# Optimization experiments

Hardware: AMD Instinct MI355X
Metric: run time of the kernel (lower is better)

## Reference

```python
import jax, jax.numpy as jnp
import numpy as np

H, KVH, HD, DM = 32, 8, 128, 4096  # attention heads, kv heads, head_dim, hidden


def _rope_tables(batch, seq, head_dim):
    # standard RoPE tables, flattened per token to match varlen layout
    inv_freq = 1.0 / (10000.0 ** (np.arange(0, head_dim, 2, dtype=np.float32) / head_dim))
    pos = np.arange(seq, dtype=np.float32)
    freqs = np.outer(pos, inv_freq)                      # [S, HD/2]
    emb = np.concatenate([freqs, freqs], axis=-1)        # [S, HD]
    cos = np.tile(np.cos(emb), (batch, 1))               # [B*S, HD]
    sin = np.tile(np.sin(emb), (batch, 1))
    return jnp.asarray(cos), jnp.asarray(sin)


def setup_inputs() -> dict:
    key = jax.random.key(0)
    k1, k2 = jax.random.split(key)
    B, S = 2, 1024
    hidden_states = jax.random.normal(k1, (B * S, DM), dtype=jnp.float32) * 0.02
    w_qkv = jax.random.normal(k2, (DM, (H + 2 * KVH) * HD), dtype=jnp.float32) * 0.02
    cos, sin = _rope_tables(B, S, HD)
    return {"hidden_states": hidden_states, "w_qkv": w_qkv, "cos": cos,
            "sin": sin, "batch_size": B, "seq_len": S}


def _rotate_half(x):
    half = x.shape[-1] // 2
    return jnp.concatenate([-x[..., half:], x[..., :half]], axis=-1)


def reference(hidden_states, w_qkv, cos, sin, batch_size, seq_len):
    B, S = batch_size, seq_len
    T = B * S
    n_rep = H // KVH
    scale = 1.0 / jnp.sqrt(jnp.asarray(HD, hidden_states.dtype))

    qkv = hidden_states @ w_qkv                           # [T, (H+2*KVH)*HD]
    q = qkv[:, : H * HD].reshape(T, H, HD)
    k = qkv[:, H * HD : (H + KVH) * HD].reshape(T, KVH, HD)
    v = qkv[:, (H + KVH) * HD :].reshape(T, KVH, HD)

    # RoPE (rotary half) on q and k
    c, s = cos[:, None, :], sin[:, None, :]
    q = q * c + _rotate_half(q) * s
    k = k * c + _rotate_half(k) * s

    # prefill SDPA branch: reshape to [B, heads, S, HD], GQA repeat on kv heads
    q = q.reshape(B, S, H, HD).transpose(0, 2, 1, 3)      # [B,H,S,HD]
    k = k.reshape(B, S, KVH, HD).transpose(0, 2, 1, 3)
    v = v.reshape(B, S, KVH, HD).transpose(0, 2, 1, 3)
    k = jnp.repeat(k, n_rep, axis=1)                      # [B,H,S,HD]
    v = jnp.repeat(v, n_rep, axis=1)

    scores = jnp.einsum("bhqd,bhkd->bhqk", q, k) * scale  # [B,H,S,S]
    causal = jnp.tril(jnp.ones((S, S), dtype=bool))
    scores = jnp.where(causal, scores, jnp.asarray(-jnp.inf, scores.dtype))
    probs = jax.nn.softmax(scores, axis=-1)
    attn = jnp.einsum("bhqk,bhkd->bhqd", probs, v)        # [B,H,S,HD]

    # postprocess_attention_output: transpose back and flatten tokens
    attn = attn.transpose(0, 2, 1, 3).reshape(T, H * HD)  # [T, H*HD]
    return attn
```

## Files before the change

### kernel.cpp

```cpp
#include <hip/hip_runtime.h>
#include <hip/hip_bf16.h>
#include <stdint.h>

constexpr int NH   = 32;
constexpr int NKVH = 8;
constexpr int HD   = 128;
constexpr int DM   = 4096;
constexpr int B    = 2;
constexpr int S    = 1024;
constexpr int T    = B * S;
constexpr int QKVN = (NH + 2 * NKVH) * HD;
constexpr int KOFF = NH * HD;
constexpr int VOFF = (NH + NKVH) * HD;

typedef float floatx4 __attribute__((ext_vector_type(4)));
typedef floatx4 floatx4_a __attribute__((may_alias));
typedef __bf16 bf16x8 __attribute__((ext_vector_type(8)));
typedef bf16x8 bf16x8_a __attribute__((may_alias));
typedef __bf16 bf16_a __attribute__((may_alias));

__device__ __forceinline__ void gload_lds16(const void* g, void* l) {
  __builtin_amdgcn_global_load_lds(
      (const __attribute__((address_space(1))) void*)g,
      (__attribute__((address_space(3))) void*)l, 16, 0, 0);
}

__global__ __launch_bounds__(256) void convert_a(const float* __restrict__ A,
                                                 __bf16* __restrict__ A16) {
  const size_t i = (size_t)(blockIdx.x * 256 + threadIdx.x) * 8;
  floatx4 v0 = *(const floatx4_a*)(A + i);
  floatx4 v1 = *(const floatx4_a*)(A + i + 4);
  bf16x8 o;
#pragma unroll
  for (int e = 0; e < 4; ++e) {
    o[e] = (__bf16)v0[e];
    o[e + 4] = (__bf16)v1[e];
  }
  *(bf16x8_a*)(A16 + i) = o;
}

__global__ __launch_bounds__(256) void transpose_w(
    const float* __restrict__ W, __bf16* __restrict__ WT) {
  __shared__ __align__(16) __bf16 ls[64][72];
  const int k0 = blockIdx.x * 64;
  const int n0 = blockIdx.y * 64;
  const int tx = threadIdx.x & 15, ty = threadIdx.x >> 4;
#pragma unroll
  for (int rr = 0; rr < 4; ++rr) {
    const int k = ty + rr * 16;
    floatx4 v = *(const floatx4_a*)(W + (size_t)(k0 + k) * QKVN + n0 + tx * 4);
#pragma unroll
    for (int e = 0; e < 4; ++e) ls[tx * 4 + e][k] = (__bf16)v[e];
  }
  __syncthreads();
#pragma unroll
  for (int it = 0; it < 2; ++it) {
    const int n = (threadIdx.x >> 3) + it * 32;
    const int c = threadIdx.x & 7;
    bf16x8 o = *(const bf16x8_a*)(&ls[n][c * 8]);
    *(bf16x8_a*)(WT + (size_t)(n0 + n) * DM + k0 + c * 8) = o;
  }
}

__global__ __launch_bounds__(256) void gemm_mfma(
    const __bf16* __restrict__ A16, const __bf16* __restrict__ W16T,
    float* __restrict__ C) {
  __shared__ __align__(16) __bf16 Asig[128 * 64];
  __shared__ __align__(16) __bf16 Bsig[128 * 64];

  const int tid = threadIdx.x;
  const int lane = tid & 63, w = tid >> 6;
  const int l15 = lane & 15, g = lane >> 4;
  const int r7 = l15 & 7;
  const int m0 = blockIdx.x * 128;
  const int n0 = blockIdx.y * 128;
  const int wrbase = (w >> 1) * 64, wcbase = (w & 1) * 64;

  const int srow = tid >> 3;
  const int sce = ((tid & 7) ^ (srow & 7)) << 3;
  const __bf16* agp = A16 + (size_t)(m0 + srow) * DM + sce;
  const __bf16* bgp = W16T + (size_t)(n0 + srow) * DM + sce;
  char* al = (char*)Asig + w * 1024;
  char* bl = (char*)Bsig + w * 1024;

  const char* Abase = (const char*)Asig + (wrbase + l15) * 128;
  const char* Bbase = (const char*)Bsig + (wcbase + l15) * 128;

  floatx4 acc[4][4];
#pragma unroll
  for (int i = 0; i < 4; ++i)
#pragma unroll
    for (int j = 0; j < 4; ++j) acc[i][j] = (floatx4){0.f, 0.f, 0.f, 0.f};

  for (int kk = 0; kk < DM; kk += 64) {
    __syncthreads();
#pragma unroll
    for (int j = 0; j < 4; ++j) {
      gload_lds16(agp + kk + (size_t)(32 * j) * DM, al + j * 4096);
      gload_lds16(bgp + kk + (size_t)(32 * j) * DM, bl + j * 4096);
    }
    __syncthreads();

#pragma unroll
    for (int kh = 0; kh < 2; ++kh) {
      const int sw = (((kh << 2) | g) ^ r7) << 4;
      bf16x8 af[4], bf[4];
#pragma unroll
      for (int i = 0; i < 4; ++i) {
        af[i] = *(const bf16x8_a*)(Abase + i * 2048 + sw);
        bf[i] = *(const bf16x8_a*)(Bbase + i * 2048 + sw);
      }
#pragma unroll
      for (int i = 0; i < 4; ++i)
#pragma unroll
        for (int j = 0; j < 4; ++j)
          acc[i][j] = __builtin_amdgcn_mfma_f32_16x16x32_bf16(af[i], bf[j],
                                                              acc[i][j], 0, 0, 0);
    }
  }

#pragma unroll
  for (int i = 0; i < 4; ++i)
#pragma unroll
    for (int j = 0; j < 4; ++j)
#pragma unroll
      for (int ri = 0; ri < 4; ++ri)
        C[(size_t)(m0 + wrbase + i * 16 + g * 4 + ri) * QKVN + n0 + wcbase +
          j * 16 + l15] = acc[i][j][ri];
}

__global__ __launch_bounds__(256) void gemm_naive(
    const float* __restrict__ A, const float* __restrict__ W,
    float* __restrict__ C) {
  __shared__ float As[16][65];
  __shared__ float Bs[16][64];
  const int tid = threadIdx.x;
  const int tx = tid & 15, ty = tid >> 4;
  const int m0 = blockIdx.y * 64, n0 = blockIdx.x * 64;
  const int sm = tid >> 2, sk4 = (tid & 3) * 4;
  const int bk = tid >> 4, bn4 = (tid & 15) * 4;
  float acc[4][4];
#pragma unroll
  for (int i = 0; i < 4; ++i)
#pragma unroll
    for (int j = 0; j < 4; ++j) acc[i][j] = 0.f;
  for (int kk = 0; kk < DM; kk += 16) {
    __syncthreads();
    floatx4 va = *(const floatx4_a*)(A + (size_t)(m0 + sm) * DM + kk + sk4);
#pragma unroll
    for (int e = 0; e < 4; ++e) As[sk4 + e][sm] = va[e];
    floatx4 vb = *(const floatx4_a*)(W + (size_t)(kk + bk) * QKVN + n0 + bn4);
    *(floatx4*)&Bs[bk][bn4] = vb;
    __syncthreads();
#pragma unroll
    for (int k = 0; k < 16; ++k) {
      float a[4], b[4];
#pragma unroll
      for (int e = 0; e < 4; ++e) a[e] = As[k][ty * 4 + e];
#pragma unroll
      for (int e = 0; e < 4; ++e) b[e] = Bs[k][tx * 4 + e];
#pragma unroll
      for (int i = 0; i < 4; ++i)
#pragma unroll
        for (int j = 0; j < 4; ++j) acc[i][j] += a[i] * b[j];
    }
  }
#pragma unroll
  for (int i = 0; i < 4; ++i)
#pragma unroll
    for (int j = 0; j < 4; ++j)
      C[(size_t)(m0 + ty * 4 + i) * QKVN + n0 + tx * 4 + j] = acc[i][j];
}

__global__ __launch_bounds__(256) void attn_mfma(
    const float* __restrict__ qkv, const float* __restrict__ cosp,
    const float* __restrict__ sinp, float* __restrict__ out) {
  __shared__ __align__(16) char Ksh[32 * 128 * 2];
  __shared__ __align__(16) char Vsh[128 * 32 * 2];
  __shared__ __align__(16) char Psh[4][16 * 32 * 2];

  const int tid = threadIdx.x;
  const int lane = tid & 63, wave = tid >> 6;
  const int raw = (int)blockIdx.x;
  const int qb_raw = raw & 63;
  const int qb = ((raw >> 8) & 1) ? (63 - qb_raw) : qb_raw;
  const int kvh = (raw >> 6) & 7;
  const int b = raw >> 9;
  const int q0 = qb * 16;
  const int h = kvh * 4 + wave;
  const int NT = (q0 + 47) >> 5;
  const float scale = 0.08838834764831845f;

  const int l15 = lane & 15, g = lane >> 4;

  bf16x8 af[4];
  {
    const size_t tok = (size_t)(b * S + q0 + l15);
    const float* qr = qkv + tok * QKVN + h * HD;
    const float* cr = cosp + tok * HD;
    const float* sr = sinp + tok * HD;
#pragma unroll
    for (int c = 0; c < 2; ++c) {
      const int d0 = c * 32 + g * 8;
      floatx4 x10 = *(const floatx4_a*)(qr + d0);
      floatx4 x11 = *(const floatx4_a*)(qr + d0 + 4);
      floatx4 x20 = *(const floatx4_a*)(qr + d0 + 64);
      floatx4 x21 = *(const floatx4_a*)(qr + d0 + 68);
      floatx4 c0 = *(const floatx4_a*)(cr + d0);
      floatx4 c1 = *(const floatx4_a*)(cr + d0 + 4);
      floatx4 s0 = *(const floatx4_a*)(sr + d0);
      floatx4 s1 = *(const floatx4_a*)(sr + d0 + 4);
      bf16x8 alo, ahi;
#pragma unroll
      for (int e = 0; e < 4; ++e) {
        alo[e] = (__bf16)((x10[e] * c0[e] - x20[e] * s0[e]) * scale);
        alo[e + 4] = (__bf16)((x11[e] * c1[e] - x21[e] * s1[e]) * scale);
        ahi[e] = (__bf16)((x20[e] * c0[e] + x10[e] * s0[e]) * scale);
        ahi[e + 4] = (__bf16)((x21[e] * c1[e] + x11[e] * s1[e]) * scale);
      }
      af[c] = alo;
      af[c + 2] = ahi;
    }
  }

  floatx4 oacc[8];
#pragma unroll
  for (int i = 0; i < 8; ++i) oacc[i] = (floatx4){0.f, 0.f, 0.f, 0.f};
  float mrow[4], lrow[4], alpha[4];
#pragma unroll
  for (int i = 0; i < 4; ++i) {
    mrow[i] = -__builtin_inff();
    lrow[i] = 0.f;
  }

  const int krow = tid >> 3, kd8 = (tid & 7) * 8;
  const int vk = tid & 31, vdb = (tid >> 5) * 16;
  const float* kbaseg = qkv + (size_t)b * S * QKVN + KOFF + kvh * HD;
  const float* vbaseg = qkv + (size_t)b * S * QKVN + VOFF + kvh * HD;
  char* pb = (char*)Psh[wave];

  for (int kt = 0; kt < NT; ++kt) {
    const int kb = kt * 32;
    __syncthreads();
    {
      const int t = kb + krow;
      const float* src = kbaseg + (size_t)t * QKVN + kd8;
      const float* crk = cosp + (size_t)(b * S + t) * HD + kd8;
      const float* srk = sinp + (size_t)(b * S + t) * HD + kd8;
      floatx4 x10 = *(const floatx4_a*)(src);
      floatx4 x11 = *(const floatx4_a*)(src + 4);
      floatx4 x20 = *(const floatx4_a*)(src + 64);
      floatx4 x21 = *(const floatx4_a*)(src + 68);
      floatx4 c0 = *(const floatx4_a*)(crk);
      floatx4 c1 = *(const floatx4_a*)(crk + 4);
      floatx4 s0 = *(const floatx4_a*)(srk);
      floatx4 s1 = *(const floatx4_a*)(srk + 4);
      bf16x8 plo, phi;
#pragma unroll
      for (int e = 0; e < 4; ++e) {
        plo[e] = (__bf16)(x10[e] * c0[e] - x20[e] * s0[e]);
        plo[e + 4] = (__bf16)(x11[e] * c1[e] - x21[e] * s1[e]);
        phi[e] = (__bf16)(x20[e] * c0[e] + x10[e] * s0[e]);
        phi[e + 4] = (__bf16)(x21[e] * c1[e] + x11[e] * s1[e]);
      }
      const int swz = (krow & 7) << 4;
      const int base = krow * 256 + kd8 * 2;
      *(bf16x8_a*)(Ksh + (base ^ swz)) = plo;
      *(bf16x8_a*)(Ksh + ((base + 128) ^ swz)) = phi;
    }
    {
      const float* src = vbaseg + (size_t)(kb + vk) * QKVN + vdb;
#pragma unroll
      for (int q4 = 0; q4 < 4; ++q4) {
        floatx4 v = *(const floatx4_a*)(src + q4 * 4);
#pragma unroll
        for (int e = 0; e < 4; ++e) {
          const int d = vdb + q4 * 4 + e;
          *(bf16_a*)(Vsh + ((d * 64 + vk * 2) ^ (((d >> 2) & 3) << 4))) =
              (__bf16)v[e];
        }
      }
    }
    __syncthreads();

    floatx4 sa0 = {0.f, 0.f, 0.f, 0.f};
    floatx4 sa1 = {0.f, 0.f, 0.f, 0.f};
    {
      const int kswz = (l15 & 7) << 4;
#pragma unroll
      for (int c = 0; c < 4; ++c) {
        bf16x8 b0 =
            *(const bf16x8_a*)(Ksh + ((l15 * 256 + c * 64 + g * 16) ^ kswz));
        bf16x8 b1 = *(const bf16x8_a*)(Ksh +
                                       (((l15 + 16) * 256 + c * 64 + g * 16) ^
                                        kswz));
        sa0 = __builtin_amdgcn_mfma_f32_16x16x32_bf16(af[c], b0, sa0, 0, 0, 0);
        sa1 = __builtin_amdgcn_mfma_f32_16x16x32_bf16(af[c], b1, sa1, 0, 0, 0);
      }
    }

    float p0a[4], p1a[4];
#pragma unroll
    for (int i = 0; i < 4; ++i) {
      const int qg = q0 + 4 * g + i;
      float s0 = sa0[i];
      float s1 = sa1[i];
      if (kb + l15 > qg) s0 = -3e38f;
      if (kb + 16 + l15 > qg) s1 = -3e38f;
      float t = fmaxf(s0, s1);
      t = fmaxf(t, __shfl_xor(t, 1));
      t = fmaxf(t, __shfl_xor(t, 2));
      t = fmaxf(t, __shfl_xor(t, 4));
      t = fmaxf(t, __shfl_xor(t, 8));
      const float mn = fmaxf(mrow[i], t);
      const float al = __expf(mrow[i] - mn);
      const float e0 = __expf(s0 - mn);
      const float e1 = __expf(s1 - mn);
      float ps = e0 + e1;
      ps += __shfl_xor(ps, 1);
      ps += __shfl_xor(ps, 2);
      ps += __shfl_xor(ps, 4);
      ps += __shfl_xor(ps, 8);
      lrow[i] = lrow[i] * al + ps;
      mrow[i] = mn;
      alpha[i] = al;
      p0a[i] = e0;
      p1a[i] = e1;
    }
#pragma unroll
    for (int df = 0; df < 8; ++df)
#pragma unroll
      for (int i = 0; i < 4; ++i) oacc[df][i] *= alpha[i];

#pragma unroll
    for (int i = 0; i < 4; ++i) {
      const int row = 4 * g + i;
      const int sw = ((row >> 1) & 3) << 4;
      *(bf16_a*)(pb + ((row * 64 + l15 * 2) ^ sw)) = (__bf16)p0a[i];
      *(bf16_a*)(pb + ((row * 64 + (16 + l15) * 2) ^ sw)) = (__bf16)p1a[i];
    }
    bf16x8 pa = *(const bf16x8_a*)(pb + ((l15 * 64 + g * 16) ^
                                         (((l15 >> 1) & 3) << 4)));

    {
      const int vswz = ((l15 >> 2) & 3) << 4;
#pragma unroll
      for (int df = 0; df < 8; ++df) {
        const int d = df * 16 + l15;
        bf16x8 vb = *(const bf16x8_a*)(Vsh + ((d * 64 + g * 16) ^ vswz));
        oacc[df] =
            __builtin_amdgcn_mfma_f32_16x16x32_bf16(pa, vb, oacc[df], 0, 0, 0);
      }
    }
  }

  float* ob = out + (size_t)(b * S + q0) * (NH * HD) + h * HD;
#pragma unroll
  for (int i = 0; i < 4; ++i) {
    const float inv = 1.f / lrow[i];
    const int row = 4 * g + i;
#pragma unroll
    for (int df = 0; df < 8; ++df)
      ob[(size_t)row * (NH * HD) + df * 16 + l15] = oacc[df][i] * inv;
  }
}

extern "C" void kernel_launch(void* const* d_in, const int* in_sizes, int n_in,
                              void* d_out, int out_size, void* d_ws,
                              size_t ws_size, hipStream_t stream) {
  const float* hidden = (const float*)d_in[0];
  const float* w_qkv = (const float*)d_in[1];
  const float* cosb = (const float*)d_in[2];
  const float* sinb = (const float*)d_in[3];
  float* out = (float*)d_out;

  char* ws = (char*)d_ws;
  float* qkv = (float*)ws;
  const size_t qkv_bytes = (size_t)T * QKVN * 4;
  const size_t wt_bytes = (size_t)QKVN * DM * 2;
  const size_t a16_bytes = (size_t)T * DM * 2;

  if (ws_size >= qkv_bytes + wt_bytes + a16_bytes) {
    __bf16* W16T = (__bf16*)(ws + qkv_bytes);
    __bf16* A16 = (__bf16*)(ws + qkv_bytes + wt_bytes);
    convert_a<<<(T * DM) / (256 * 8), 256, 0, stream>>>(hidden, A16);
    transpose_w<<<dim3(DM / 64, QKVN / 64), 256, 0, stream>>>(w_qkv, W16T);
    gemm_mfma<<<dim3(T / 128, QKVN / 128), 256, 0, stream>>>(A16, W16T, qkv);
  } else {
    gemm_naive<<<dim3(QKVN / 64, T / 64), 256, 0, stream>>>(hidden, w_qkv,
                                                            qkv);
  }
  attn_mfma<<<dim3(B * NKVH * (S / 16)), 256, 0, stream>>>(qkv, cosb, sinb,
                                                           out);
}
```

Baseline: 435.1 us.

## Precompute RoPE'd bf16 Q/K/V tiles and DMA them into attention with 64-key tiles

Adds prep_q and prep_kv kernels that apply RoPE, scale Q, convert to bf16 and write K and V in pre-swizzled, pre-transposed tile layouts. The attention kernel now streams these tiles straight into LDS with global_load_lds instead of recomputing RoPE and conversion for every query block, and it doubles the KV tile to 64 keys. This removes redundant fp32 loads and conversions repeated across query blocks, at the cost of two extra launches and extra workspace traffic. The naive GEMM fallback is dropped, so the code now assumes the workspace is large enough, and the scratch buffers reuse the weight and activation conversion regions.

```diff
diff --git a/kernel.cpp b/kernel.cpp
--- a/kernel.cpp
+++ b/kernel.cpp
@@ -12,6 +12,9 @@
 constexpr int QKVN = (NH + 2 * NKVH) * HD;
 constexpr int KOFF = NH * HD;
 constexpr int VOFF = (NH + NKVH) * HD;
+constexpr int KVB  = 64;
+constexpr int NKT  = S / KVB;
+constexpr int TILE_B = KVB * HD * 2;
 
 typedef float floatx4 __attribute__((ext_vector_type(4)));
 typedef floatx4 floatx4_a __attribute__((may_alias));
@@ -129,55 +132,120 @@
           j * 16 + l15] = acc[i][j][ri];
 }
 
-__global__ __launch_bounds__(256) void gemm_naive(
-    const float* __restrict__ A, const float* __restrict__ W,
-    float* __restrict__ C) {
-  __shared__ float As[16][65];
-  __shared__ float Bs[16][64];
+__global__ __launch_bounds__(256) void prep_q(const float* __restrict__ qkv,
+                                              const float* __restrict__ cosp,
+                                              const float* __restrict__ sinp,
+                                              __bf16* __restrict__ Qr) {
+  const int idx = blockIdx.x * 256 + threadIdx.x;
+  const int d0 = (idx & 7) * 8;
+  const int hidx = idx >> 3;
+  const int h = hidx & (NH - 1);
+  const int tok = hidx >> 5;
+  const float scale = 0.08838834764831845f;
+
+  const float* q = qkv + (size_t)tok * QKVN + h * HD;
+  const float* cr = cosp + (size_t)tok * HD + d0;
+  const float* sr = sinp + (size_t)tok * HD + d0;
+  floatx4 x10 = *(const floatx4_a*)(q + d0);
+  floatx4 x11 = *(const floatx4_a*)(q + d0 + 4);
+  floatx4 x20 = *(const floatx4_a*)(q + d0 + 64);
+  floatx4 x21 = *(const floatx4_a*)(q + d0 + 68);
+  floatx4 c0 = *(const floatx4_a*)(cr);
+  floatx4 c1 = *(const floatx4_a*)(cr + 4);
+  floatx4 s0 = *(const floatx4_a*)(sr);
+  floatx4 s1 = *(const floatx4_a*)(sr + 4);
+  bf16x8 lo, hi;
+#pragma unroll
+  for (int e = 0; e < 4; ++e) {
+    lo[e] = (__bf16)((x10[e] * c0[e] - x20[e] * s0[e]) * scale);
+    lo[e + 4] = (__bf16)((x11[e] * c1[e] - x21[e] * s1[e]) * scale);
+    hi[e] = (__bf16)((x20[e] * c0[e] + x10[e] * s0[e]) * scale);
+    hi[e + 4] = (__bf16)((x21[e] * c1[e] + x11[e] * s1[e]) * scale);
+  }
+  __bf16* o = Qr + (size_t)tok * (NH * HD) + h * HD + d0;
+  *(bf16x8_a*)(o) = lo;
+  *(bf16x8_a*)(o + 64) = hi;
+}
+
+__global__ __launch_bounds__(256) void prep_kv(const float* __restrict__ qkv,
+                                               const float* __restrict__ cosp,
+                                               const float* __restrict__ sinp,
+                                               char* __restrict__ Kr,
+                                               char* __restrict__ Vr) {
+  __shared__ __align__(16) __bf16 vls[128][72];
+  const int bid = (int)blockIdx.x;
+  const int kt = bid & (NKT - 1);
+  const int kvh = (bid >> 4) & (NKVH - 1);
+  const int b = bid >> 7;
   const int tid = threadIdx.x;
-  const int tx = tid & 15, ty = tid >> 4;
-  const int m0 = blockIdx.y * 64, n0 = blockIdx.x * 64;
-  const int sm = tid >> 2, sk4 = (tid & 3) * 4;
-  const int bk = tid >> 4, bn4 = (tid & 15) * 4;
-  float acc[4][4];
-#pragma unroll
-  for (int i = 0; i < 4; ++i)
-#pragma unroll
-    for (int j = 0; j < 4; ++j) acc[i][j] = 0.f;
-  for (int kk = 0; kk < DM; kk += 16) {
-    __syncthreads();
-    floatx4 va = *(const floatx4_a*)(A + (size_t)(m0 + sm) * DM + kk + sk4);
-#pragma unroll
-    for (int e = 0; e < 4; ++e) As[sk4 + e][sm] = va[e];
-    floatx4 vb = *(const floatx4_a*)(W + (size_t)(kk + bk) * QKVN + n0 + bn4);
-    *(floatx4*)&Bs[bk][bn4] = vb;
-    __syncthreads();
-#pragma unroll
-    for (int k = 0; k < 16; ++k) {
-      float a[4], b[4];
-#pragma unroll
-      for (int e = 0; e < 4; ++e) a[e] = As[k][ty * 4 + e];
-#pragma unroll
-      for (int e = 0; e < 4; ++e) b[e] = Bs[k][tx * 4 + e];
-#pragma unroll
-      for (int i = 0; i < 4; ++i)
-#pragma unroll
-        for (int j = 0; j < 4; ++j) acc[i][j] += a[i] * b[j];
-    }
-  }
-#pragma unroll
-  for (int i = 0; i < 4; ++i)
-#pragma unroll
-    for (int j = 0; j < 4; ++j)
-      C[(size_t)(m0 + ty * 4 + i) * QKVN + n0 + tx * 4 + j] = acc[i][j];
+  const int key = tid >> 2;
+  const int tok = kt * KVB + key;
+  const size_t trow = (size_t)(b * S + tok);
+  char* kr_tile = Kr + (size_t)((b * NKVH + kvh) * NKT + kt) * TILE_B;
+  char* vr_tile = Vr + (size_t)((b * NKVH + kvh) * NKT + kt) * TILE_B;
+
+  {
+    const int d0 = (tid & 3) * 16;
+    const float* kp = qkv + trow * QKVN + KOFF + kvh * HD;
+    const float* cr = cosp + trow * HD + d0;
+    const float* sr = sinp + trow * HD + d0;
+    bf16x8 lo[2], hi[2];
+#pragma unroll
+    for (int m = 0; m < 2; ++m) {
+      floatx4 x10 = *(const floatx4_a*)(kp + d0 + m * 8);
+      floatx4 x11 = *(const floatx4_a*)(kp + d0 + m * 8 + 4);
+      floatx4 x20 = *(const floatx4_a*)(kp + d0 + m * 8 + 64);
+      floatx4 x21 = *(const floatx4_a*)(kp + d0 + m * 8 + 68);
+      floatx4 c0 = *(const floatx4_a*)(cr + m * 8);
+      floatx4 c1 = *(const floatx4_a*)(cr + m * 8 + 4);
+      floatx4 s0 = *(const floatx4_a*)(sr + m * 8);
+      floatx4 s1 = *(const floatx4_a*)(sr + m * 8 + 4);
+#pragma unroll
+      for (int e = 0; e < 4; ++e) {
+        lo[m][e] = (__bf16)(x10[e] * c0[e] - x20[e] * s0[e]);
+        lo[m][e + 4] = (__bf16)(x11[e] * c1[e] - x21[e] * s1[e]);
+        hi[m][e] = (__bf16)(x20[e] * c0[e] + x10[e] * s0[e]);
+        hi[m][e + 4] = (__bf16)(x21[e] * c1[e] + x11[e] * s1[e]);
+      }
+    }
+    const int swz = (key & 7) << 4;
+    const int base = key * 256 + d0 * 2;
+#pragma unroll
+    for (int m = 0; m < 2; ++m) {
+      *(bf16x8_a*)(kr_tile + ((base + m * 16) ^ swz)) = lo[m];
+      *(bf16x8_a*)(kr_tile + ((base + 128 + m * 16) ^ swz)) = hi[m];
+    }
+  }
+
+  {
+    const int e0 = (tid & 3) * 32;
+    const float* vp = qkv + trow * QKVN + VOFF + kvh * HD;
+#pragma unroll
+    for (int m = 0; m < 8; ++m) {
+      floatx4 v = *(const floatx4_a*)(vp + e0 + m * 4);
+#pragma unroll
+      for (int e = 0; e < 4; ++e) vls[e0 + m * 4 + e][key] = (__bf16)v[e];
+    }
+  }
+  __syncthreads();
+  {
+    const int d = tid >> 1;
+    const int h2 = tid & 1;
+    const int vswz = (d & 7) << 4;
+#pragma unroll
+    for (int j = 0; j < 4; ++j) {
+      bf16x8 o = *(const bf16x8_a*)(&vls[d][h2 * 32 + j * 8]);
+      *(bf16x8_a*)(vr_tile + ((d * 128 + h2 * 64 + j * 16) ^ vswz)) = o;
+    }
+  }
 }
 
 __global__ __launch_bounds__(256) void attn_mfma(
-    const float* __restrict__ qkv, const float* __restrict__ cosp,
-    const float* __restrict__ sinp, float* __restrict__ out) {
-  __shared__ __align__(16) char Ksh[32 * 128 * 2];
-  __shared__ __align__(16) char Vsh[128 * 32 * 2];
-  __shared__ __align__(16) char Psh[4][16 * 32 * 2];
+    const __bf16* __restrict__ Qr, const char* __restrict__ Kr,
+    const char* __restrict__ Vr, float* __restrict__ out) {
+  __shared__ __align__(16) char Ksh[TILE_B];
+  __shared__ __align__(16) char Vsh[TILE_B];
+  __shared__ __align__(16) char Psh[4][16 * KVB * 2];
 
   const int tid = threadIdx.x;
   const int lane = tid & 63, wave = tid >> 6;
@@ -188,39 +256,15 @@
   const int b = raw >> 9;
   const int q0 = qb * 16;
   const int h = kvh * 4 + wave;
-  const int NT = (q0 + 47) >> 5;
-  const float scale = 0.08838834764831845f;
-
+  const int NT = (q0 + 79) >> 6;
   const int l15 = lane & 15, g = lane >> 4;
 
   bf16x8 af[4];
   {
-    const size_t tok = (size_t)(b * S + q0 + l15);
-    const float* qr = qkv + tok * QKVN + h * HD;
-    const float* cr = cosp + tok * HD;
-    const float* sr = sinp + tok * HD;
-#pragma unroll
-    for (int c = 0; c < 2; ++c) {
-      const int d0 = c * 32 + g * 8;
-      floatx4 x10 = *(const floatx4_a*)(qr + d0);
-      floatx4 x11 = *(const floatx4_a*)(qr + d0 + 4);
-      floatx4 x20 = *(const floatx4_a*)(qr + d0 + 64);
-      floatx4 x21 = *(const floatx4_a*)(qr + d0 + 68);
-      floatx4 c0 = *(const floatx4_a*)(cr + d0);
-      floatx4 c1 = *(const floatx4_a*)(cr + d0 + 4);
-      floatx4 s0 = *(const floatx4_a*)(sr + d0);
-      floatx4 s1 = *(const floatx4_a*)(sr + d0 + 4);
-      bf16x8 alo, ahi;
-#pragma unroll
-      for (int e = 0; e < 4; ++e) {
-        alo[e] = (__bf16)((x10[e] * c0[e] - x20[e] * s0[e]) * scale);
-        alo[e + 4] = (__bf16)((x11[e] * c1[e] - x21[e] * s1[e]) * scale);
-        ahi[e] = (__bf16)((x20[e] * c0[e] + x10[e] * s0[e]) * scale);
-        ahi[e + 4] = (__bf16)((x21[e] * c1[e] + x11[e] * s1[e]) * scale);
-      }
-      af[c] = alo;
-      af[c + 2] = ahi;
-    }
+    const __bf16* qr = Qr + (size_t)(b * S + q0 + l15) * (NH * HD) + h * HD;
+#pragma unroll
+    for (int c = 0; c < 4; ++c)
+      af[c] = *(const bf16x8_a*)(qr + c * 32 + g * 8);
   }
 
   floatx4 oacc[8];
@@ -233,81 +277,50 @@
     lrow[i] = 0.f;
   }
 
-  const int krow = tid >> 3, kd8 = (tid & 7) * 8;
-  const int vk = tid & 31, vdb = (tid >> 5) * 16;
-  const float* kbaseg = qkv + (size_t)b * S * QKVN + KOFF + kvh * HD;
-  const float* vbaseg = qkv + (size_t)b * S * QKVN + VOFF + kvh * HD;
+  const char* kbase = Kr + (size_t)((b * NKVH + kvh) * NKT) * TILE_B;
+  const char* vbase = Vr + (size_t)((b * NKVH + kvh) * NKT) * TILE_B;
   char* pb = (char*)Psh[wave];
+  const int dmaoff = wave * 1024 + (lane << 4);
+  const int ldsoff = wave * 1024;
+  const int swz = (l15 & 7) << 4;
 
   for (int kt = 0; kt < NT; ++kt) {
-    const int kb = kt * 32;
     __syncthreads();
-    {
-      const int t = kb + krow;
-      const float* src = kbaseg + (size_t)t * QKVN + kd8;
-      const float* crk = cosp + (size_t)(b * S + t) * HD + kd8;
-      const float* srk = sinp + (size_t)(b * S + t) * HD + kd8;
-      floatx4 x10 = *(const floatx4_a*)(src);
-      floatx4 x11 = *(const floatx4_a*)(src + 4);
-      floatx4 x20 = *(const floatx4_a*)(src + 64);
-      floatx4 x21 = *(const floatx4_a*)(src + 68);
-      floatx4 c0 = *(const floatx4_a*)(crk);
-      floatx4 c1 = *(const floatx4_a*)(crk + 4);
-      floatx4 s0 = *(const floatx4_a*)(srk);
-      floatx4 s1 = *(const floatx4_a*)(srk + 4);
-      bf16x8 plo, phi;
-#pragma unroll
-      for (int e = 0; e < 4; ++e) {
-        plo[e] = (__bf16)(x10[e] * c0[e] - x20[e] * s0[e]);
-        plo[e + 4] = (__bf16)(x11[e] * c1[e] - x21[e] * s1[e]);
-        phi[e] = (__bf16)(x20[e] * c0[e] + x10[e] * s0[e]);
-        phi[e + 4] = (__bf16)(x21[e] * c1[e] + x11[e] * s1[e]);
+    const char* ks = kbase + kt * TILE_B;
+    const char* vs = vbase + kt * TILE_B;
+#pragma unroll
+    for (int j = 0; j < 4; ++j)
+      gload_lds16(ks + j * 4096 + dmaoff, Ksh + j * 4096 + ldsoff);
+#pragma unroll
+    for (int j = 0; j < 4; ++j)
+      gload_lds16(vs + j * 4096 + dmaoff, Vsh + j * 4096 + ldsoff);
+    __syncthreads();
+
+    floatx4 sa[4];
+#pragma unroll
+    for (int f = 0; f < 4; ++f) sa[f] = (floatx4){0.f, 0.f, 0.f, 0.f};
+#pragma unroll
+    for (int c = 0; c < 4; ++c) {
+#pragma unroll
+      for (int f = 0; f < 4; ++f) {
+        bf16x8 bk = *(const bf16x8_a*)(
+            Ksh + (((f * 16 + l15) * 256 + c * 64 + g * 16) ^ swz));
+        sa[f] = __builtin_amdgcn_mfma_f32_16x16x32_bf16(af[c], bk, sa[f], 0, 0,
+                                                        0);
       }
-      const int swz = (krow & 7) << 4;
-      const int base = krow * 256 + kd8 * 2;
-      *(bf16x8_a*)(Ksh + (base ^ swz)) = plo;
-      *(bf16x8_a*)(Ksh + ((base + 128) ^ swz)) = phi;
-    }
-    {
-      const float* src = vbaseg + (size_t)(kb + vk) * QKVN + vdb;
-#pragma unroll
-      for (int q4 = 0; q4 < 4; ++q4) {
-        floatx4 v = *(const floatx4_a*)(src + q4 * 4);
-#pragma unroll
-        for (int e = 0; e < 4; ++e) {
-          const int d = vdb + q4 * 4 + e;
-          *(bf16_a*)(Vsh + ((d * 64 + vk * 2) ^ (((d >> 2) & 3) << 4))) =
-              (__bf16)v[e];
-        }
-      }
-    }
-    __syncthreads();
-
-    floatx4 sa0 = {0.f, 0.f, 0.f, 0.f};
-    floatx4 sa1 = {0.f, 0.f, 0.f, 0.f};
-    {
-      const int kswz = (l15 & 7) << 4;
-#pragma unroll
-      for (int c = 0; c < 4; ++c) {
-        bf16x8 b0 =
-            *(const bf16x8_a*)(Ksh + ((l15 * 256 + c * 64 + g * 16) ^ kswz));
-        bf16x8 b1 = *(const bf16x8_a*)(Ksh +
-                                       (((l15 + 16) * 256 + c * 64 + g * 16) ^
-                                        kswz));
-        sa0 = __builtin_amdgcn_mfma_f32_16x16x32_bf16(af[c], b0, sa0, 0, 0, 0);
-        sa1 = __builtin_amdgcn_mfma_f32_16x16x32_bf16(af[c], b1, sa1, 0, 0, 0);
-      }
-    }
-
-    float p0a[4], p1a[4];
+    }
+
+    const int kb = kt * KVB;
+    float p[4][4];
 #pragma unroll
     for (int i = 0; i < 4; ++i) {
       const int qg = q0 + 4 * g + i;
-      float s0 = sa0[i];
-      float s1 = sa1[i];
+      float s0 = sa[0][i], s1 = sa[1][i], s2 = sa[2][i], s3 = sa[3][i];
       if (kb + l15 > qg) s0 = -3e38f;
       if (kb + 16 + l15 > qg) s1 = -3e38f;
-      float t = fmaxf(s0, s1);
+      if (kb + 32 + l15 > qg) s2 = -3e38f;
+      if (kb + 48 + l15 > qg) s3 = -3e38f;
+      float t = fmaxf(fmaxf(s0, s1), fmaxf(s2, s3));
       t = fmaxf(t, __shfl_xor(t, 1));
       t = fmaxf(t, __shfl_xor(t, 2));
       t = fmaxf(t, __shfl_xor(t, 4));
@@ -316,7 +329,9 @@
       const float al = __expf(mrow[i] - mn);
       const float e0 = __expf(s0 - mn);
       const float e1 = __expf(s1 - mn);
-      float ps = e0 + e1;
+      const float e2 = __expf(s2 - mn);
+      const float e3 = __expf(s3 - mn);
+      float ps = (e0 + e1) + (e2 + e3);
       ps += __shfl_xor(ps, 1);
       ps += __shfl_xor(ps, 2);
       ps += __shfl_xor(ps, 4);
@@ -324,8 +339,7 @@
       lrow[i] = lrow[i] * al + ps;
       mrow[i] = mn;
       alpha[i] = al;
-      p0a[i] = e0;
-      p1a[i] = e1;
+      p[i][0] = e0; p[i][1] = e1; p[i][2] = e2; p[i][3] = e3;
     }
 #pragma unroll
     for (int df = 0; df < 8; ++df)
@@ -335,22 +349,24 @@
 #pragma unroll
     for (int i = 0; i < 4; ++i) {
       const int row = 4 * g + i;
-      const int sw = ((row >> 1) & 3) << 4;
-      *(bf16_a*)(pb + ((row * 64 + l15 * 2) ^ sw)) = (__bf16)p0a[i];
-      *(bf16_a*)(pb + ((row * 64 + (16 + l15) * 2) ^ sw)) = (__bf16)p1a[i];
-    }
-    bf16x8 pa = *(const bf16x8_a*)(pb + ((l15 * 64 + g * 16) ^
-                                         (((l15 >> 1) & 3) << 4)));
-
-    {
-      const int vswz = ((l15 >> 2) & 3) << 4;
-#pragma unroll
-      for (int df = 0; df < 8; ++df) {
-        const int d = df * 16 + l15;
-        bf16x8 vb = *(const bf16x8_a*)(Vsh + ((d * 64 + g * 16) ^ vswz));
-        oacc[df] =
-            __builtin_amdgcn_mfma_f32_16x16x32_bf16(pa, vb, oacc[df], 0, 0, 0);
-      }
+      const int sw = (row & 7) << 4;
+#pragma unroll
+      for (int f = 0; f < 4; ++f)
+        *(bf16_a*)(pb + ((row * 128 + (f * 16 + l15) * 2) ^ sw)) =
+            (__bf16)p[i][f];
+    }
+    bf16x8 pa0 = *(const bf16x8_a*)(pb + ((l15 * 128 + g * 16) ^ swz));
+    bf16x8 pa1 = *(const bf16x8_a*)(pb + ((l15 * 128 + 64 + g * 16) ^ swz));
+
+#pragma unroll
+    for (int df = 0; df < 8; ++df) {
+      const int d = df * 16 + l15;
+      bf16x8 v0 = *(const bf16x8_a*)(Vsh + ((d * 128 + g * 16) ^ swz));
+      bf16x8 v1 = *(const bf16x8_a*)(Vsh + ((d * 128 + 64 + g * 16) ^ swz));
+      oacc[df] =
+          __builtin_amdgcn_mfma_f32_16x16x32_bf16(pa0, v0, oacc[df], 0, 0, 0);
+      oacc[df] =
+          __builtin_amdgcn_mfma_f32_16x16x32_bf16(pa1, v1, oacc[df], 0, 0, 0);
     }
   }
 
@@ -375,21 +391,19 @@
   float* out = (float*)d_out;
 
   char* ws = (char*)d_ws;
-  float* qkv = (float*)ws;
   const size_t qkv_bytes = (size_t)T * QKVN * 4;
   const size_t wt_bytes = (size_t)QKVN * DM * 2;
-  const size_t a16_bytes = (size_t)T * DM * 2;
-
-  if (ws_size >= qkv_bytes + wt_bytes + a16_bytes) {
-    __bf16* W16T = (__bf16*)(ws + qkv_bytes);
-    __bf16* A16 = (__bf16*)(ws + qkv_bytes + wt_bytes);
-    convert_a<<<(T * DM) / (256 * 8), 256, 0, stream>>>(hidden, A16);
-    transpose_w<<<dim3(DM / 64, QKVN / 64), 256, 0, stream>>>(w_qkv, W16T);
-    gemm_mfma<<<dim3(T / 128, QKVN / 128), 256, 0, stream>>>(A16, W16T, qkv);
-  } else {
-    gemm_naive<<<dim3(QKVN / 64, T / 64), 256, 0, stream>>>(hidden, w_qkv,
-                                                            qkv);
-  }
-  attn_mfma<<<dim3(B * NKVH * (S / 16)), 256, 0, stream>>>(qkv, cosb, sinb,
-                                                           out);
-}
+  float* qkv = (float*)ws;
+  __bf16* W16T = (__bf16*)(ws + qkv_bytes);
+  __bf16* A16 = (__bf16*)(ws + qkv_bytes + wt_bytes);
+  __bf16* Qr = (__bf16*)(ws + qkv_bytes);
+  char* Kr = (char*)(ws + qkv_bytes + wt_bytes);
+  char* Vr = Kr + (size_t)B * NKVH * NKT * TILE_B;
+
+  convert_a<<<(T * DM) / (256 * 8), 256, 0, stream>>>(hidden, A16);
+  transpose_w<<<dim3(DM / 64, QKVN / 64), 256, 0, stream>>>(w_qkv, W16T);
+  gemm_mfma<<<dim3(T / 128, QKVN / 128), 256, 0, stream>>>(A16, W16T, qkv);
+  prep_q<<<(T * NH * 8) / 256, 256, 0, stream>>>(qkv, cosb, sinb, Qr);
+  prep_kv<<<B * NKVH * NKT, 256, 0, stream>>>(qkv, cosb, sinb, Kr, Vr);
+  attn_mfma<<<dim3(B * NKVH * (S / 16)), 256, 0, stream>>>(Qr, Kr, Vr, out);
+}
```

Result: faster. 397.5 us (-8.7%).
